# Optimization experiments

Measured on AMD Instinct MI355X. Metric: run time of the kernel, lower is better.

The kernel has to match this reference:

```python
import jax, jax.numpy as jnp
import numpy as np

N_PTS = 800000
PLANE = 512
FDIM = 16


def setup_inputs() -> dict:
    key = jax.random.key(0)
    k1, k2 = jax.random.split(key)
    x = jax.random.uniform(k1, (N_PTS, 3), dtype=jnp.float32)
    # learned tri-plane features, init U(-0.01, 0.01) as in init_parameters
    fm = jax.random.uniform(k2, (3, PLANE, PLANE, FDIM), dtype=jnp.float32,
                            minval=-0.01, maxval=0.01)
    return {"x": x, "fm": fm}


def reference(x, fm):
    # x: [N,3] in [0,1]; fm: [3,H,W,C] tri-plane textures
    N = x.shape[0]
    _, H, W, C = fm.shape
    # decompose xyz into the three plane uv coords: (yz), (xz), (xy)
    dx = jnp.stack([x[:, (1, 2)], x[:, (0, 2)], x[:, (0, 1)]], axis=0)  # [3,N,2]
    # nvdiffrast texture convention: u along W, v along H, texel centers at (i+0.5)/W
    u = dx[..., 0] * W - 0.5  # [3,N]
    v = dx[..., 1] * H - 0.5
    i0f = jnp.floor(u)
    j0f = jnp.floor(v)
    fu = u - i0f  # bilinear fractions, [3,N]
    fv = v - j0f
    i0 = jnp.clip(i0f.astype(jnp.int32), 0, W - 1)  # clamp boundary mode
    i1 = jnp.clip(i0f.astype(jnp.int32) + 1, 0, W - 1)
    j0 = jnp.clip(j0f.astype(jnp.int32), 0, H - 1)
    j1 = jnp.clip(j0f.astype(jnp.int32) + 1, 0, H - 1)
    p = jnp.arange(3)[:, None]  # plane index, broadcasts against [3,N]
    t00 = fm[p, j0, i0]  # [3,N,C]
    t01 = fm[p, j0, i1]
    t10 = fm[p, j1, i0]
    t11 = fm[p, j1, i1]
    w00 = ((1.0 - fv) * (1.0 - fu))[..., None]
    w01 = ((1.0 - fv) * fu)[..., None]
    w10 = (fv * (1.0 - fu))[..., None]
    w11 = (fv * fu)[..., None]
    enc = w00 * t00 + w01 * t01 + w10 * t10 + w11 * t11  # [3,N,C]
    # permute(1,2,0,3).view(N, 3*C) on [3,N,1,C] == transpose to [N,3,C] then flatten
    return enc.transpose(1, 0, 2).reshape(N, 3 * C)
```

## Files before the change

kernel.cpp:

```cpp
#include <hip/hip_runtime.h>
#include <hip/hip_bf16.h>


#define N_PTS 800000
#define PLANE 512
#define FDIM  16
#define FM_ELEMS (3 * PLANE * PLANE * FDIM)
#define FMH_BYTES (FM_ELEMS * 2)
#define NBINS 4096
#define CAP 256
#define OVF_CAP 131072
#define MAIN_UNITS (NBINS * CAP)
#define GATHER_UNITS (MAIN_UNITS + OVF_CAP)
#define GATHER2_THREADS (GATHER_UNITS * 8)
#define GATHER2_BLOCKS (GATHER2_THREADS / 256)

#define WS_FMH_OFF 0
#define WS_CNT_OFF FMH_BYTES
#define WS_OVFCNT_OFF (WS_CNT_OFF + NBINS * 4)
#define WS_SLOT_OFF (WS_OVFCNT_OFF + 16)
#define WS_OVF_OFF (WS_SLOT_OFF + MAIN_UNITS * 16)
#define WS_TOTAL (WS_OVF_OFF + OVF_CAP * 16)

#define GATHER_THREADS (N_PTS * 8)
#define PT_BLOCKS (N_PTS / 256)
#define TOTAL_F32 (N_PTS * 48)

typedef _Float16 half2v __attribute__((ext_vector_type(2)));
typedef _Float16 half4v __attribute__((ext_vector_type(4)));
typedef float    float2v __attribute__((ext_vector_type(2)));

__global__ __launch_bounds__(256) void convert_fp16_zero_kernel(
    const float* __restrict__ fm, _Float16* __restrict__ fmh,
    unsigned* __restrict__ cntz)
{
    unsigned t = blockIdx.x * blockDim.x + threadIdx.x;
    if (cntz != (unsigned*)0 && blockIdx.x == 0) {
        for (unsigned z = threadIdx.x; z < (unsigned)(NBINS + 1); z += 256u)
            cntz[z] = 0u;
    }
    if (t >= (unsigned)(FM_ELEMS / 4)) return;
    float4 v = ((const float4*)fm)[t];
    half4v h;
    h.x = (_Float16)v.x; h.y = (_Float16)v.y;
    h.z = (_Float16)v.z; h.w = (_Float16)v.w;
    ((half4v*)fmh)[t] = h;
}

__device__ __forceinline__ unsigned spread4(unsigned v)
{
    return (v & 1u) | ((v & 2u) << 2) | ((v & 4u) << 4) | ((v & 8u) << 6);
}

__device__ __forceinline__ unsigned morton_key(float x0, float x1, float x2)
{
    int ix = min(max((int)(x0 * 16.0f), 0), 15);
    int iy = min(max((int)(x1 * 16.0f), 0), 15);
    int iz = min(max((int)(x2 * 16.0f), 0), 15);
    return spread4((unsigned)ix) | (spread4((unsigned)iy) << 1)
         | (spread4((unsigned)iz) << 2);
}

__global__ __launch_bounds__(256) void scatter_direct_kernel(
    const float* __restrict__ x, unsigned* __restrict__ cnt,
    unsigned* __restrict__ ovfcnt,
    float4* __restrict__ slots, float4* __restrict__ ovf)
{
    unsigned t = blockIdx.x * blockDim.x + threadIdx.x;
    if (t >= (unsigned)N_PTS) return;
    float x0 = x[3u * t + 0u];
    float x1 = x[3u * t + 1u];
    float x2 = x[3u * t + 2u];
    unsigned key = morton_key(x0, x1, x2);
    unsigned pos = atomicAdd(&cnt[key], 1u);
    float4 rec;
    rec.x = x0; rec.y = x1; rec.z = x2; rec.w = __uint_as_float(t);
    if (pos < (unsigned)CAP) {
        slots[key * CAP + pos] = rec;
    } else {
        unsigned o = atomicAdd(ovfcnt, 1u);
        if (o < (unsigned)OVF_CAP) ovf[o] = rec;
    }
}

__global__ __launch_bounds__(256) void trimip_fp16_bucket_kernel(
    const float4* __restrict__ slots,
    const float4* __restrict__ ovf,
    const unsigned* __restrict__ cnt,
    const unsigned* __restrict__ ovfcnt,
    const _Float16* __restrict__ fmh,
    float* __restrict__ out)
{
    unsigned bid = blockIdx.x;
    unsigned swz = (bid & 7u) * (GATHER2_BLOCKS / 8u) + (bid >> 3);
    unsigned t = swz * 256u + threadIdx.x;

    unsigned c2 = t & 7u;
    unsigned u  = t >> 3;

    float4 rec;
    if (u < (unsigned)MAIN_UNITS) {
        unsigned bin  = u >> 8;
        unsigned slot = u & 255u;
        unsigned c = cnt[bin];
        if (c > (unsigned)CAP) c = (unsigned)CAP;
        if (slot >= c) return;
        rec = slots[u];
    } else {
        unsigned ou = u - (unsigned)MAIN_UNITS;
        unsigned oc = *ovfcnt;
        if (oc > (unsigned)OVF_CAP) oc = (unsigned)OVF_CAP;
        if (ou >= oc) return;
        rec = ovf[ou];
    }

    float x0 = rec.x, x1 = rec.y, x2 = rec.z;
    unsigned n = __float_as_uint(rec.w);
    if (n >= (unsigned)N_PTS) return;

    float ua[3] = {x1, x0, x0};
    float va[3] = {x2, x2, x1};

    float fu[3], fv[3];
    unsigned o00[3], o01[3], o10[3], o11[3];

#pragma unroll
    for (int p = 0; p < 3; ++p) {
        float u_ = ua[p] * (float)PLANE - 0.5f;
        float v_ = va[p] * (float)PLANE - 0.5f;
        float i0f = floorf(u_);
        float j0f = floorf(v_);
        fu[p] = u_ - i0f;
        fv[p] = v_ - j0f;

        int i0 = (int)i0f;
        int j0 = (int)j0f;
        int i1 = min(max(i0 + 1, 0), PLANE - 1);
        int j1 = min(max(j0 + 1, 0), PLANE - 1);
        i0 = min(max(i0, 0), PLANE - 1);
        j0 = min(max(j0, 0), PLANE - 1);

        unsigned pb = (unsigned)p * (PLANE * PLANE * FDIM) + 2u * c2;
        o00[p] = pb + (unsigned)(j0 * PLANE + i0) * FDIM;
        o01[p] = pb + (unsigned)(j0 * PLANE + i1) * FDIM;
        o10[p] = pb + (unsigned)(j1 * PLANE + i0) * FDIM;
        o11[p] = pb + (unsigned)(j1 * PLANE + i1) * FDIM;
    }

    half2v h00[3], h01[3], h10[3], h11[3];
#pragma unroll
    for (int p = 0; p < 3; ++p) {
        h00[p] = *(const half2v*)(fmh + o00[p]);
        h01[p] = *(const half2v*)(fmh + o01[p]);
        h10[p] = *(const half2v*)(fmh + o10[p]);
        h11[p] = *(const half2v*)(fmh + o11[p]);
    }

    float2v* ob = (float2v*)out + (size_t)n * 24u + c2;
#pragma unroll
    for (int p = 0; p < 3; ++p) {
        float2v r;
        {
            float t00 = (float)h00[p].x, t01 = (float)h01[p].x;
            float t10 = (float)h10[p].x, t11 = (float)h11[p].x;
            float r0 = t00 + fu[p] * (t01 - t00);
            float r1 = t10 + fu[p] * (t11 - t10);
            r.x = r0 + fv[p] * (r1 - r0);
        }
        {
            float t00 = (float)h00[p].y, t01 = (float)h01[p].y;
            float t10 = (float)h10[p].y, t11 = (float)h11[p].y;
            float r0 = t00 + fu[p] * (t01 - t00);
            float r1 = t10 + fu[p] * (t11 - t10);
            r.y = r0 + fv[p] * (r1 - r0);
        }
        __builtin_nontemporal_store(r, ob + (unsigned)p * 8u);
    }
}

__global__ __launch_bounds__(256) void trimip_fp16_fused_kernel(
    const float* __restrict__ x,
    const _Float16* __restrict__ fmh,
    float* __restrict__ out)
{
    unsigned t = blockIdx.x * blockDim.x + threadIdx.x;
    if (t >= (unsigned)GATHER_THREADS) return;

    unsigned c2 = t & 7u;
    unsigned n  = t >> 3;

    const float* xr = x + 3u * n;
    float x0 = xr[0], x1 = xr[1], x2 = xr[2];

    float ua[3] = {x1, x0, x0};
    float va[3] = {x2, x2, x1};

    float fu[3], fv[3];
    unsigned o00[3], o01[3], o10[3], o11[3];

#pragma unroll
    for (int p = 0; p < 3; ++p) {
        float u = ua[p] * (float)PLANE - 0.5f;
        float v = va[p] * (float)PLANE - 0.5f;
        float i0f = floorf(u);
        float j0f = floorf(v);
        fu[p] = u - i0f;
        fv[p] = v - j0f;

        int i0 = (int)i0f;
        int j0 = (int)j0f;
        int i1 = min(max(i0 + 1, 0), PLANE - 1);
        int j1 = min(max(j0 + 1, 0), PLANE - 1);
        i0 = min(max(i0, 0), PLANE - 1);
        j0 = min(max(j0, 0), PLANE - 1);

        unsigned pb = (unsigned)p * (PLANE * PLANE * FDIM) + 2u * c2;
        o00[p] = pb + (unsigned)(j0 * PLANE + i0) * FDIM;
        o01[p] = pb + (unsigned)(j0 * PLANE + i1) * FDIM;
        o10[p] = pb + (unsigned)(j1 * PLANE + i0) * FDIM;
        o11[p] = pb + (unsigned)(j1 * PLANE + i1) * FDIM;
    }

    half2v h00[3], h01[3], h10[3], h11[3];
#pragma unroll
    for (int p = 0; p < 3; ++p) {
        h00[p] = *(const half2v*)(fmh + o00[p]);
        h01[p] = *(const half2v*)(fmh + o01[p]);
        h10[p] = *(const half2v*)(fmh + o10[p]);
        h11[p] = *(const half2v*)(fmh + o11[p]);
    }

    float2v* ob = (float2v*)out + (size_t)n * 24u + c2;
#pragma unroll
    for (int p = 0; p < 3; ++p) {
        float2v r;
        {
            float t00 = (float)h00[p].x, t01 = (float)h01[p].x;
            float t10 = (float)h10[p].x, t11 = (float)h11[p].x;
            float r0 = t00 + fu[p] * (t01 - t00);
            float r1 = t10 + fu[p] * (t11 - t10);
            r.x = r0 + fv[p] * (r1 - r0);
        }
        {
            float t00 = (float)h00[p].y, t01 = (float)h01[p].y;
            float t10 = (float)h10[p].y, t11 = (float)h11[p].y;
            float r0 = t00 + fu[p] * (t01 - t00);
            float r1 = t10 + fu[p] * (t11 - t10);
            r.y = r0 + fv[p] * (r1 - r0);
        }
        __builtin_nontemporal_store(r, ob + (unsigned)p * 8u);
    }
}

__global__ __launch_bounds__(256) void trimip_f32_kernel(
    const float* __restrict__ x,
    const float* __restrict__ fm,
    float* __restrict__ out)
{
    unsigned t = blockIdx.x * blockDim.x + threadIdx.x;
    if (t >= (unsigned)TOTAL_F32) return;

    unsigned c    = t & 15u;
    unsigned unit = t >> 4;
    unsigned n    = unit / 3u;
    unsigned p    = unit - n * 3u;

    unsigned iu = (p == 0u) ? 1u : 0u;
    unsigned iv = (p == 2u) ? 1u : 2u;

    float a = x[n * 3u + iu];
    float b = x[n * 3u + iv];

    float u = a * (float)PLANE - 0.5f;
    float v = b * (float)PLANE - 0.5f;
    float i0f = floorf(u);
    float j0f = floorf(v);
    float fu = u - i0f;
    float fv = v - j0f;

    int i0 = (int)i0f;
    int j0 = (int)j0f;
    int i1 = min(max(i0 + 1, 0), PLANE - 1);
    int j1 = min(max(j0 + 1, 0), PLANE - 1);
    i0 = min(max(i0, 0), PLANE - 1);
    j0 = min(max(j0, 0), PLANE - 1);

    const float* base = fm + (size_t)p * (PLANE * PLANE * FDIM);
    float t00 = base[((size_t)(j0 * PLANE + i0)) * FDIM + c];
    float t01 = base[((size_t)(j0 * PLANE + i1)) * FDIM + c];
    float t10 = base[((size_t)(j1 * PLANE + i0)) * FDIM + c];
    float t11 = base[((size_t)(j1 * PLANE + i1)) * FDIM + c];

    float r0 = t00 + fu * (t01 - t00);
    float r1 = t10 + fu * (t11 - t10);
    float r  = r0 + fv * (r1 - r0);

    __builtin_nontemporal_store(r, &out[t]);
}

extern "C" void kernel_launch(void* const* d_in, const int* in_sizes, int n_in,
                              void* d_out, int out_size, void* d_ws, size_t ws_size,
                              hipStream_t stream)
{
    const float* x  = (const float*)d_in[0];
    const float* fm = (const float*)d_in[1];
    float* out      = (float*)d_out;

    if (ws_size >= (size_t)WS_TOTAL) {
        char* ws = (char*)d_ws;
        _Float16* fmh   = (_Float16*)(ws + WS_FMH_OFF);
        unsigned* cnt   = (unsigned*)(ws + WS_CNT_OFF);
        unsigned* ovfc  = (unsigned*)(ws + WS_OVFCNT_OFF);
        float4*   slots = (float4*)(ws + WS_SLOT_OFF);
        float4*   ovf   = (float4*)(ws + WS_OVF_OFF);

        convert_fp16_zero_kernel<<<FM_ELEMS / 4 / 256, 256, 0, stream>>>(fm, fmh, cnt);
        scatter_direct_kernel<<<PT_BLOCKS, 256, 0, stream>>>(x, cnt, ovfc, slots, ovf);
        trimip_fp16_bucket_kernel<<<GATHER2_BLOCKS, 256, 0, stream>>>(
            slots, ovf, cnt, ovfc, fmh, out);
    } else if (ws_size >= (size_t)FMH_BYTES) {
        _Float16* fmh = (_Float16*)d_ws;
        convert_fp16_zero_kernel<<<FM_ELEMS / 4 / 256, 256, 0, stream>>>(fm, fmh, (unsigned*)0);
        trimip_fp16_fused_kernel<<<(GATHER_THREADS + 255) / 256, 256, 0, stream>>>(x, fmh, out);
    } else {
        trimip_f32_kernel<<<(TOTAL_F32 + 255) / 256, 256, 0, stream>>>(x, fm, out);
    }
}
```

Baseline: 297.6 us.

## Merge fp16 conversion and point scatter into one launch, memset counters

Fuses the feature-map fp16 conversion and the Morton-bin scatter into a single kernel with block-range dispatch, so the two independent phases run concurrently instead of in two serialized launches. Counter zeroing moves to a hipMemsetAsync issued beforehand. The gather kernel's output stores change from nontemporal to ordinary stores. This saves a launch and a phase boundary, but adds a memset node, and dropping the nontemporal hint may increase cache pollution from the large output.

```diff
diff --git a/kernel.cpp b/kernel.cpp
--- a/kernel.cpp
+++ b/kernel.cpp
@@ -15,6 +15,10 @@
 #define GATHER2_THREADS (GATHER_UNITS * 8)
 #define GATHER2_BLOCKS (GATHER2_THREADS / 256)
 
+#define CONV_BLOCKS (FM_ELEMS / 4 / 256)
+#define PT_BLOCKS (N_PTS / 256)
+#define MERGED_BLOCKS (CONV_BLOCKS + PT_BLOCKS)
+
 #define WS_FMH_OFF 0
 #define WS_CNT_OFF FMH_BYTES
 #define WS_OVFCNT_OFF (WS_CNT_OFF + NBINS * 4)
@@ -23,29 +27,11 @@
 #define WS_TOTAL (WS_OVF_OFF + OVF_CAP * 16)
 
 #define GATHER_THREADS (N_PTS * 8)
-#define PT_BLOCKS (N_PTS / 256)
 #define TOTAL_F32 (N_PTS * 48)
 
 typedef _Float16 half2v __attribute__((ext_vector_type(2)));
 typedef _Float16 half4v __attribute__((ext_vector_type(4)));
 typedef float    float2v __attribute__((ext_vector_type(2)));
-
-__global__ __launch_bounds__(256) void convert_fp16_zero_kernel(
-    const float* __restrict__ fm, _Float16* __restrict__ fmh,
-    unsigned* __restrict__ cntz)
-{
-    unsigned t = blockIdx.x * blockDim.x + threadIdx.x;
-    if (cntz != (unsigned*)0 && blockIdx.x == 0) {
-        for (unsigned z = threadIdx.x; z < (unsigned)(NBINS + 1); z += 256u)
-            cntz[z] = 0u;
-    }
-    if (t >= (unsigned)(FM_ELEMS / 4)) return;
-    float4 v = ((const float4*)fm)[t];
-    half4v h;
-    h.x = (_Float16)v.x; h.y = (_Float16)v.y;
-    h.z = (_Float16)v.z; h.w = (_Float16)v.w;
-    ((half4v*)fmh)[t] = h;
-}
 
 __device__ __forceinline__ unsigned spread4(unsigned v)
 {
@@ -61,25 +47,35 @@
          | (spread4((unsigned)iz) << 2);
 }
 
-__global__ __launch_bounds__(256) void scatter_direct_kernel(
+__global__ __launch_bounds__(256) void convert_scatter_kernel(
+    const float* __restrict__ fm, _Float16* __restrict__ fmh,
     const float* __restrict__ x, unsigned* __restrict__ cnt,
     unsigned* __restrict__ ovfcnt,
     float4* __restrict__ slots, float4* __restrict__ ovf)
 {
-    unsigned t = blockIdx.x * blockDim.x + threadIdx.x;
-    if (t >= (unsigned)N_PTS) return;
-    float x0 = x[3u * t + 0u];
-    float x1 = x[3u * t + 1u];
-    float x2 = x[3u * t + 2u];
-    unsigned key = morton_key(x0, x1, x2);
-    unsigned pos = atomicAdd(&cnt[key], 1u);
-    float4 rec;
-    rec.x = x0; rec.y = x1; rec.z = x2; rec.w = __uint_as_float(t);
-    if (pos < (unsigned)CAP) {
-        slots[key * CAP + pos] = rec;
+    if (blockIdx.x < (unsigned)CONV_BLOCKS) {
+        unsigned t = blockIdx.x * 256u + threadIdx.x;
+        float4 v = ((const float4*)fm)[t];
+        half4v h;
+        h.x = (_Float16)v.x; h.y = (_Float16)v.y;
+        h.z = (_Float16)v.z; h.w = (_Float16)v.w;
+        ((half4v*)fmh)[t] = h;
     } else {
-        unsigned o = atomicAdd(ovfcnt, 1u);
-        if (o < (unsigned)OVF_CAP) ovf[o] = rec;
+        unsigned t = (blockIdx.x - (unsigned)CONV_BLOCKS) * 256u + threadIdx.x;
+        if (t >= (unsigned)N_PTS) return;
+        float x0 = x[3u * t + 0u];
+        float x1 = x[3u * t + 1u];
+        float x2 = x[3u * t + 2u];
+        unsigned key = morton_key(x0, x1, x2);
+        unsigned pos = atomicAdd(&cnt[key], 1u);
+        float4 rec;
+        rec.x = x0; rec.y = x1; rec.z = x2; rec.w = __uint_as_float(t);
+        if (pos < (unsigned)CAP) {
+            slots[key * (unsigned)CAP + pos] = rec;
+        } else {
+            unsigned o = atomicAdd(ovfcnt, 1u);
+            if (o < (unsigned)OVF_CAP) ovf[o] = rec;
+        }
     }
 }
 
@@ -174,8 +170,20 @@
             float r1 = t10 + fu[p] * (t11 - t10);
             r.y = r0 + fv[p] * (r1 - r0);
         }
-        __builtin_nontemporal_store(r, ob + (unsigned)p * 8u);
-    }
+        ob[(unsigned)p * 8u] = r;
+    }
+}
+
+__global__ __launch_bounds__(256) void convert_fp16_kernel(
+    const float* __restrict__ fm, _Float16* __restrict__ fmh)
+{
+    unsigned t = blockIdx.x * blockDim.x + threadIdx.x;
+    if (t >= (unsigned)(FM_ELEMS / 4)) return;
+    float4 v = ((const float4*)fm)[t];
+    half4v h;
+    h.x = (_Float16)v.x; h.y = (_Float16)v.y;
+    h.z = (_Float16)v.z; h.w = (_Float16)v.w;
+    ((half4v*)fmh)[t] = h;
 }
 
 __global__ __launch_bounds__(256) void trimip_fp16_fused_kernel(
@@ -314,13 +322,14 @@
         float4*   slots = (float4*)(ws + WS_SLOT_OFF);
         float4*   ovf   = (float4*)(ws + WS_OVF_OFF);
 
-        convert_fp16_zero_kernel<<<FM_ELEMS / 4 / 256, 256, 0, stream>>>(fm, fmh, cnt);
-        scatter_direct_kernel<<<PT_BLOCKS, 256, 0, stream>>>(x, cnt, ovfc, slots, ovf);
+        hipMemsetAsync(cnt, 0, (NBINS + 1) * sizeof(unsigned), stream);
+        convert_scatter_kernel<<<MERGED_BLOCKS, 256, 0, stream>>>(
+            fm, fmh, x, cnt, ovfc, slots, ovf);
         trimip_fp16_bucket_kernel<<<GATHER2_BLOCKS, 256, 0, stream>>>(
             slots, ovf, cnt, ovfc, fmh, out);
     } else if (ws_size >= (size_t)FMH_BYTES) {
         _Float16* fmh = (_Float16*)d_ws;
-        convert_fp16_zero_kernel<<<FM_ELEMS / 4 / 256, 256, 0, stream>>>(fm, fmh, (unsigned*)0);
+        convert_fp16_kernel<<<CONV_BLOCKS, 256, 0, stream>>>(fm, fmh);
         trimip_fp16_fused_kernel<<<(GATHER_THREADS + 255) / 256, 256, 0, stream>>>(x, fmh, out);
     } else {
         trimip_f32_kernel<<<(TOTAL_F32 + 255) / 256, 256, 0, stream>>>(x, fm, out);
```

Result: slower. 328.8 us (+10.5%).
